# Kernel tuning notes

Hardware: AMD Instinct MI355X
Metric: run time of the kernel (lower is better)

Reference implementation:

```python
import jax, jax.numpy as jnp
import numpy as np

B, S, E, H = 2, 2048, 1024, 16
D = E // H  # head_dim = 64


def setup_inputs() -> dict:
    key = jax.random.key(0)
    ks = jax.random.split(key, 6)
    sc = 1.0 / np.sqrt(D)
    return {
        "x": jax.random.normal(ks[0], (B, S, E), dtype=jnp.float32),
        "Wq": jax.random.normal(ks[1], (D, D), dtype=jnp.float32) * sc,
        "Wk": jax.random.normal(ks[2], (D, D), dtype=jnp.float32) * sc,
        "Wv": jax.random.normal(ks[3], (D, D), dtype=jnp.float32) * sc,
        "Wo": jax.random.normal(ks[4], (E, E), dtype=jnp.float32) * (1.0 / np.sqrt(E)),
        "bo": jnp.zeros((E,), dtype=jnp.float32),
    }


def reference(x, Wq, Wk, Wv, Wo, bo):
    b, s, e = x.shape
    # split into heads: (B, H, S, D)
    xh = x.reshape(b, s, H, D).transpose(0, 2, 1, 3)
    # per-head linear projections (weights SHARED across heads); torch Linear: x @ W^T
    q = jnp.einsum('bhsd,ed->bhse', xh, Wq)
    k = jnp.einsum('bhsd,ed->bhse', xh, Wk)
    v = jnp.einsum('bhsd,ed->bhse', xh, Wv)
    # full attention matrix (B, H, S, S) — faithful to the naive original
    energy = jnp.einsum('bhqd,bhkd->bhqk', q, k)
    attn = jax.nn.softmax(energy / jnp.sqrt(jnp.asarray(D, x.dtype)), axis=-1)
    out = jnp.einsum('bhqk,bhkd->bhqd', attn, v)
    out = out.transpose(0, 2, 1, 3).reshape(b, s, e)
    return out @ Wo.T + bo
```

## Files before the change

### kernel.cpp

```cpp
#include <hip/hip_runtime.h>
#include <hip/hip_bf16.h>

#define B 2
#define S 2048
#define E 1024
#define H 16
#define D 64

typedef unsigned short ushort_t;
typedef __attribute__((ext_vector_type(8))) short bf16x8;
typedef __attribute__((ext_vector_type(4))) float f32x4;
typedef __attribute__((ext_vector_type(16))) float f32x16;

static __device__ __forceinline__ ushort_t f2bf(float f) {
    union { float f; unsigned u; } v; v.f = f;
    unsigned r = v.u + 0x7fffu + ((v.u >> 16) & 1u);
    return (ushort_t)(r >> 16);
}

#define MFMA(a, b, c)   __builtin_amdgcn_mfma_f32_16x16x32_bf16((a), (b), (c), 0, 0, 0)
#define MFMA32(a, b, c) __builtin_amdgcn_mfma_f32_32x32x16_bf16((a), (b), (c), 0, 0, 0)
#define PACKBF(hi, lo) __builtin_amdgcn_perm((hi), (lo), 0x07060302u)

__global__ __launch_bounds__(256) void cvt_w(
    const float* __restrict__ Wq, const float* __restrict__ Wk, const float* __restrict__ Wv,
    const float* __restrict__ Wo,
    ushort_t* __restrict__ wqb, ushort_t* __restrict__ wkb, ushort_t* __restrict__ wvb,
    ushort_t* __restrict__ wob)
{
    int gid = blockIdx.x, t = threadIdx.x;
    if (gid < 1024) {
        int i = gid * 1024 + t * 4;
        float4 f = *(const float4*)(Wo + i);
        ushort4 u; u.x = f2bf(f.x); u.y = f2bf(f.y); u.z = f2bf(f.z); u.w = f2bf(f.w);
        *(ushort4*)(wob + i) = u;
    } else {
        int idx = (gid - 1024) * 1024 + t * 4;
        int which = idx >> 12, off = idx & 4095;
        const float* src = (which == 0) ? Wq : (which == 1) ? Wk : Wv;
        ushort_t* dst    = (which == 0) ? wqb : (which == 1) ? wkb : wvb;
        float sc = (which == 0) ? 0.18033688011112042f : 1.0f;
        float4 f = *(const float4*)(src + off);
        ushort4 u; u.x = f2bf(f.x * sc); u.y = f2bf(f.y * sc);
        u.z = f2bf(f.z * sc); u.w = f2bf(f.w * sc);
        *(ushort4*)(dst + off) = u;
    }
}

__global__ __launch_bounds__(256) void qkv_proj(
    const float* __restrict__ x,
    const ushort_t* __restrict__ wq, const ushort_t* __restrict__ wk, const ushort_t* __restrict__ wv,
    ushort_t* __restrict__ q, ushort_t* __restrict__ k, ushort_t* __restrict__ vT)
{
    __shared__ ushort_t Xs[64][72];
    __shared__ ushort_t Wqs[64][72], Wks[64][72], Wvs[64][72];
    int t = threadIdx.x;
    int bh = blockIdx.y, b = bh >> 4, h = bh & 15;
    int s0 = blockIdx.x * 64;

    {
        int i = t >> 2, d0 = (t & 3) * 16;
        const float* xp = x + ((size_t)(b * S + s0 + i)) * E + h * D + d0;
        #pragma unroll
        for (int c = 0; c < 16; c += 4) {
            float4 f = *(const float4*)(xp + c);
            Xs[i][d0 + c + 0] = f2bf(f.x); Xs[i][d0 + c + 1] = f2bf(f.y);
            Xs[i][d0 + c + 2] = f2bf(f.z); Xs[i][d0 + c + 3] = f2bf(f.w);
        }
    }
    {
        int e = t >> 2, d0 = (t & 3) * 16;
        *(bf16x8*)&Wqs[e][d0]     = *(const bf16x8*)(wq + e * 64 + d0);
        *(bf16x8*)&Wqs[e][d0 + 8] = *(const bf16x8*)(wq + e * 64 + d0 + 8);
        *(bf16x8*)&Wks[e][d0]     = *(const bf16x8*)(wk + e * 64 + d0);
        *(bf16x8*)&Wks[e][d0 + 8] = *(const bf16x8*)(wk + e * 64 + d0 + 8);
        *(bf16x8*)&Wvs[e][d0]     = *(const bf16x8*)(wv + e * 64 + d0);
        *(bf16x8*)&Wvs[e][d0 + 8] = *(const bf16x8*)(wv + e * 64 + d0 + 8);
    }
    __syncthreads();

    int w = t >> 6, lane = t & 63, m = lane & 15, quad = lane >> 4;
    bf16x8 a0 = *(bf16x8*)&Xs[16 * w + m][quad * 8];
    bf16x8 a1 = *(bf16x8*)&Xs[16 * w + m][32 + quad * 8];
    f32x4 cq[4], ck[4], cv[4];
    #pragma unroll
    for (int nt = 0; nt < 4; nt++) { cq[nt] = (f32x4)0.f; ck[nt] = (f32x4)0.f; cv[nt] = (f32x4)0.f; }
    #pragma unroll
    for (int nt = 0; nt < 4; nt++) {
        bf16x8 b0, b1;
        b0 = *(bf16x8*)&Wqs[nt * 16 + m][quad * 8]; b1 = *(bf16x8*)&Wqs[nt * 16 + m][32 + quad * 8];
        cq[nt] = MFMA(a0, b0, cq[nt]); cq[nt] = MFMA(a1, b1, cq[nt]);
        b0 = *(bf16x8*)&Wks[nt * 16 + m][quad * 8]; b1 = *(bf16x8*)&Wks[nt * 16 + m][32 + quad * 8];
        ck[nt] = MFMA(a0, b0, ck[nt]); ck[nt] = MFMA(a1, b1, ck[nt]);
        b0 = *(bf16x8*)&Wvs[nt * 16 + m][quad * 8]; b1 = *(bf16x8*)&Wvs[nt * 16 + m][32 + quad * 8];
        cv[nt] = MFMA(a0, b0, cv[nt]); cv[nt] = MFMA(a1, b1, cv[nt]);
    }
    size_t base = (size_t)bh * S + s0;
    #pragma unroll
    for (int nt = 0; nt < 4; nt++)
        #pragma unroll
        for (int r = 0; r < 4; r++) {
            size_t idx = (base + 16 * w + quad * 4 + r) * D + nt * 16 + m;
            q[idx] = f2bf(cq[nt][r]);
            k[idx] = f2bf(ck[nt][r]);
        }
    __syncthreads();
    #pragma unroll
    for (int nt = 0; nt < 4; nt++)
        #pragma unroll
        for (int r = 0; r < 4; r++)
            Wvs[nt * 16 + m][16 * w + quad * 4 + r] = f2bf(cv[nt][r]);
    __syncthreads();
    {
        int d0 = t >> 2, sc = (t & 3) * 16;
        ushort_t* vp = vT + ((size_t)bh * D + d0) * S + s0 + sc;
        *(bf16x8*)(vp)     = *(bf16x8*)&Wvs[d0][sc];
        *(bf16x8*)(vp + 8) = *(bf16x8*)&Wvs[d0][sc + 8];
    }
}

__global__ __launch_bounds__(256) void flash_attn(
    const ushort_t* __restrict__ q, const ushort_t* __restrict__ k,
    const ushort_t* __restrict__ vT, ushort_t* __restrict__ ao)
{
    __shared__ ushort_t Ks[2][64][72];
    __shared__ ushort_t Vt[2][64][72];
    int t = threadIdx.x;
    int bh = blockIdx.y, b = bh >> 4, h = bh & 15;
    int q0 = blockIdx.x * 128;
    int w = t >> 6, lane = t & 63, l31 = lane & 31, half = lane >> 5;

    const ushort_t* qb = q + ((size_t)bh * S + q0) * D;
    const ushort_t* kb = k + (size_t)bh * S * D;
    const ushort_t* vb = vT + (size_t)bh * D * S;

    bf16x8 qf[4];
    {
        const ushort_t* qp = qb + (size_t)(w * 32 + l31) * D + half * 8;
        #pragma unroll
        for (int c = 0; c < 4; c++) qf[c] = *(const bf16x8*)(qp + c * 16);
    }

    f32x16 o0 = (f32x16)0.f, o1 = (f32x16)0.f;
    float2 ls2 = make_float2(0.f, 0.f);

    int sr = t >> 2, scc = (t & 3) * 16;
    bf16x8 kp0, kp1, vp0, vp1;

    {
        const ushort_t* kp = kb + (size_t)sr * D + scc;
        const ushort_t* vp = vb + (size_t)sr * S + scc;
        kp0 = *(const bf16x8*)(kp);     kp1 = *(const bf16x8*)(kp + 8);
        vp0 = *(const bf16x8*)(vp);     vp1 = *(const bf16x8*)(vp + 8);
        *(bf16x8*)&Ks[0][sr][scc]     = kp0;
        *(bf16x8*)&Ks[0][sr][scc + 8] = kp1;
        *(bf16x8*)&Vt[0][sr][scc]     = vp0;
        *(bf16x8*)&Vt[0][sr][scc + 8] = vp1;
    }
    __syncthreads();
    {
        const ushort_t* kp = kb + (size_t)(64 + sr) * D + scc;
        const ushort_t* vp = vb + (size_t)sr * S + 64 + scc;
        kp0 = *(const bf16x8*)(kp);     kp1 = *(const bf16x8*)(kp + 8);
        vp0 = *(const bf16x8*)(vp);     vp1 = *(const bf16x8*)(vp + 8);
    }

    const int NT = S / 64;
    for (int it = 0; it < NT; it++) {
        int p = it & 1;
        if (it + 1 < NT) {
            *(bf16x8*)&Ks[1 - p][sr][scc]     = kp0;
            *(bf16x8*)&Ks[1 - p][sr][scc + 8] = kp1;
            *(bf16x8*)&Vt[1 - p][sr][scc]     = vp0;
            *(bf16x8*)&Vt[1 - p][sr][scc + 8] = vp1;
        }
        if (it + 2 < NT) {
            int k0n = (it + 2) * 64;
            const ushort_t* kp = kb + (size_t)(k0n + sr) * D + scc;
            const ushort_t* vp = vb + (size_t)sr * S + k0n + scc;
            kp0 = *(const bf16x8*)(kp);     kp1 = *(const bf16x8*)(kp + 8);
            vp0 = *(const bf16x8*)(vp);     vp1 = *(const bf16x8*)(vp + 8);
        }

        union { unsigned u[4]; bf16x8 v; } pa[4];
        #pragma unroll
        for (int st = 0; st < 2; st++) {
            f32x16 e = (f32x16)0.f;
            #pragma unroll
            for (int c = 0; c < 4; c++) {
                bf16x8 ka = *(bf16x8*)&Ks[p][st * 32 + l31][c * 16 + half * 8];
                e = MFMA32(ka, qf[c], e);
            }
            unsigned pt[16];
            #pragma unroll
            for (int r = 0; r < 16; r += 2) {
                float pe0 = __builtin_amdgcn_exp2f(e[r]);
                float pe1 = __builtin_amdgcn_exp2f(e[r + 1]);
                ls2.x += pe0; ls2.y += pe1;
                pt[r]     = __float_as_uint(pe0);
                pt[r + 1] = __float_as_uint(pe1);
            }
            #pragma unroll
            for (int c2 = 0; c2 < 2; c2++) {
                int rb = c2 * 8;
                unsigned dA = PACKBF(pt[rb + 1], pt[rb + 0]);
                unsigned dB = PACKBF(pt[rb + 3], pt[rb + 2]);
                unsigned dC = PACKBF(pt[rb + 5], pt[rb + 4]);
                unsigned dD = PACKBF(pt[rb + 7], pt[rb + 6]);
                unsigned x1 = (unsigned)__shfl_xor((int)(half ? dA : dC), 32, 64);
                unsigned x2 = (unsigned)__shfl_xor((int)(half ? dB : dD), 32, 64);
                int kc = st * 2 + c2;
                pa[kc].u[0] = half ? x1 : dA;
                pa[kc].u[1] = half ? x2 : dB;
                pa[kc].u[2] = half ? dC : x1;
                pa[kc].u[3] = half ? dD : x2;
            }
        }

        #pragma unroll
        for (int kc = 0; kc < 4; kc++) {
            bf16x8 vf0 = *(bf16x8*)&Vt[p][l31][kc * 16 + half * 8];
            bf16x8 vf1 = *(bf16x8*)&Vt[p][32 + l31][kc * 16 + half * 8];
            o0 = MFMA32(pa[kc].v, vf0, o0);
            o1 = MFMA32(pa[kc].v, vf1, o1);
        }
        __syncthreads();
    }

    float lsum = ls2.x + ls2.y;
    float lfull = lsum + __shfl_xor(lsum, 32, 64);
    float inv = 1.001953125f / lfull;
    #pragma unroll
    for (int reg = 0; reg < 16; reg++) {
        int qrow = (reg & 3) + 8 * (reg >> 2) + 4 * half;
        float li = __shfl(inv, qrow, 64);
        int srow = q0 + w * 32 + qrow;
        size_t base = ((size_t)(b * S + srow)) * E + h * D + l31;
        ao[base]      = f2bf(o0[reg] * li);
        ao[base + 32] = f2bf(o1[reg] * li);
    }
}

__global__ __launch_bounds__(256) void out_proj(
    const ushort_t* __restrict__ A, const ushort_t* __restrict__ Wob,
    const float* __restrict__ bo, float* __restrict__ Y)
{
    __shared__ ushort_t As[2][128][72];
    __shared__ ushort_t Ws[2][64][72];
    int t = threadIdx.x;
    int n0 = blockIdx.x * 64, m0 = blockIdx.y * 128;
    int w = t >> 6, lane = t & 63, m = lane & 15, quad = lane >> 4;
    f32x4 acc[2][4];
    #pragma unroll
    for (int u = 0; u < 2; u++)
        #pragma unroll
        for (int nt = 0; nt < 4; nt++) acc[u][nt] = (f32x4)0.f;

    int ar = t >> 1, ac = (t & 1) * 32;
    int wr = t >> 2, wc = (t & 3) * 16;
    const ushort_t* apb = A + (size_t)(m0 + ar) * E + ac;
    const ushort_t* wpb = Wob + (size_t)(n0 + wr) * E + wc;

    bf16x8 arg[4], wrg[2];
    {
        #pragma unroll
        for (int i = 0; i < 4; i++) *(bf16x8*)&As[0][ar][ac + 8 * i] = *(const bf16x8*)(apb + 8 * i);
        *(bf16x8*)&Ws[0][wr][wc]     = *(const bf16x8*)(wpb);
        *(bf16x8*)&Ws[0][wr][wc + 8] = *(const bf16x8*)(wpb + 8);
    }
    __syncthreads();
    {
        #pragma unroll
        for (int i = 0; i < 4; i++) arg[i] = *(const bf16x8*)(apb + 64 + 8 * i);
        wrg[0] = *(const bf16x8*)(wpb + 64);
        wrg[1] = *(const bf16x8*)(wpb + 64 + 8);
    }

    const int KT = E / 64;
    for (int ks = 0; ks < KT; ks++) {
        int p = ks & 1;
        if (ks + 1 < KT) {
            #pragma unroll
            for (int i = 0; i < 4; i++) *(bf16x8*)&As[1 - p][ar][ac + 8 * i] = arg[i];
            *(bf16x8*)&Ws[1 - p][wr][wc]     = wrg[0];
            *(bf16x8*)&Ws[1 - p][wr][wc + 8] = wrg[1];
        }
        if (ks + 2 < KT) {
            int off = (ks + 2) * 64;
            #pragma unroll
            for (int i = 0; i < 4; i++) arg[i] = *(const bf16x8*)(apb + off + 8 * i);
            wrg[0] = *(const bf16x8*)(wpb + off);
            wrg[1] = *(const bf16x8*)(wpb + off + 8);
        }
        #pragma unroll
        for (int h2 = 0; h2 < 2; h2++) {
            bf16x8 af[2];
            af[0] = *(bf16x8*)&As[p][w * 32 + m][h2 * 32 + quad * 8];
            af[1] = *(bf16x8*)&As[p][w * 32 + 16 + m][h2 * 32 + quad * 8];
            #pragma unroll
            for (int nt = 0; nt < 4; nt++) {
                bf16x8 bfr = *(bf16x8*)&Ws[p][nt * 16 + m][h2 * 32 + quad * 8];
                acc[0][nt] = MFMA(af[0], bfr, acc[0][nt]);
                acc[1][nt] = MFMA(af[1], bfr, acc[1][nt]);
            }
        }
        __syncthreads();
    }
    #pragma unroll
    for (int u = 0; u < 2; u++)
        #pragma unroll
        for (int nt = 0; nt < 4; nt++)
            #pragma unroll
            for (int r = 0; r < 4; r++) {
                int row = m0 + w * 32 + u * 16 + quad * 4 + r;
                int col = n0 + nt * 16 + m;
                Y[(size_t)row * E + col] = acc[u][nt][r] + bo[col];
            }
}

extern "C" void kernel_launch(void* const* d_in, const int* in_sizes, int n_in,
                              void* d_out, int out_size, void* d_ws, size_t ws_size,
                              hipStream_t stream)
{
    const float* x  = (const float*)d_in[0];
    const float* Wq = (const float*)d_in[1];
    const float* Wk = (const float*)d_in[2];
    const float* Wv = (const float*)d_in[3];
    const float* Wo = (const float*)d_in[4];
    const float* bo = (const float*)d_in[5];
    float* Y = (float*)d_out;

    const size_t n = (size_t)B * H * S * D;
    ushort_t* qw  = (ushort_t*)d_ws;
    ushort_t* kw  = qw + n;
    ushort_t* vTw = kw + n;
    ushort_t* ao  = vTw + n;
    ushort_t* wob = ao + n;
    ushort_t* wqb = wob + (size_t)E * E;
    ushort_t* wkb = wqb + D * D;
    ushort_t* wvb = wkb + D * D;

    cvt_w<<<dim3(1024 + 12), 256, 0, stream>>>(Wq, Wk, Wv, Wo, wqb, wkb, wvb, wob);
    qkv_proj<<<dim3(S / 64, B * H), 256, 0, stream>>>(x, wqb, wkb, wvb, qw, kw, vTw);
    flash_attn<<<dim3(S / 128, B * H), 256, 0, stream>>>(qw, kw, vTw, ao);
    out_proj<<<dim3(E / 64, (B * S) / 128), 256, 0, stream>>>(ao, wob, bo, Y);
}
```

Measured before the change: 152.2 us.

## Restructure QKV projection: weights in registers, two seq tiles per block, vector stores

The QKV projection kernel now keeps the three weight matrices as MFMA A-operands in registers and streams two 64-row sequence tiles per block, swapping the operand roles so each lane writes four contiguous q/k elements with ushort4 stores instead of scalar ones. X is loaded and converted with 16-byte LDS writes, and V is transposed through a dedicated LDS buffer. The grid is halved, which amortizes the weight loads but reduces parallelism and adds extra barriers per tile. The projection is a small part of total time next to attention and the output projection.

```diff
diff --git a/kernel.cpp b/kernel.cpp
--- a/kernel.cpp
+++ b/kernel.cpp
@@ -16,6 +16,15 @@
     union { float f; unsigned u; } v; v.f = f;
     unsigned r = v.u + 0x7fffu + ((v.u >> 16) & 1u);
     return (ushort_t)(r >> 16);
+}
+
+static __device__ __forceinline__ bf16x8 load_cvt8(const float* p) {
+    float4 f0 = *(const float4*)(p);
+    float4 f1 = *(const float4*)(p + 4);
+    union { ushort_t s[8]; bf16x8 v; } u;
+    u.s[0] = f2bf(f0.x); u.s[1] = f2bf(f0.y); u.s[2] = f2bf(f0.z); u.s[3] = f2bf(f0.w);
+    u.s[4] = f2bf(f1.x); u.s[5] = f2bf(f1.y); u.s[6] = f2bf(f1.z); u.s[7] = f2bf(f1.w);
+    return u.v;
 }
 
 #define MFMA(a, b, c)   __builtin_amdgcn_mfma_f32_16x16x32_bf16((a), (b), (c), 0, 0, 0)
@@ -52,70 +61,70 @@
     const ushort_t* __restrict__ wq, const ushort_t* __restrict__ wk, const ushort_t* __restrict__ wv,
     ushort_t* __restrict__ q, ushort_t* __restrict__ k, ushort_t* __restrict__ vT)
 {
+    __shared__ ushort_t Ws3[3][64][72];
     __shared__ ushort_t Xs[64][72];
-    __shared__ ushort_t Wqs[64][72], Wks[64][72], Wvs[64][72];
+    __shared__ ushort_t Vls[64][72];
     int t = threadIdx.x;
     int bh = blockIdx.y, b = bh >> 4, h = bh & 15;
-    int s0 = blockIdx.x * 64;
-
-    {
-        int i = t >> 2, d0 = (t & 3) * 16;
-        const float* xp = x + ((size_t)(b * S + s0 + i)) * E + h * D + d0;
-        #pragma unroll
-        for (int c = 0; c < 16; c += 4) {
-            float4 f = *(const float4*)(xp + c);
-            Xs[i][d0 + c + 0] = f2bf(f.x); Xs[i][d0 + c + 1] = f2bf(f.y);
-            Xs[i][d0 + c + 2] = f2bf(f.z); Xs[i][d0 + c + 3] = f2bf(f.w);
-        }
-    }
+    int s00 = blockIdx.x * 128;
+
     {
         int e = t >> 2, d0 = (t & 3) * 16;
-        *(bf16x8*)&Wqs[e][d0]     = *(const bf16x8*)(wq + e * 64 + d0);
-        *(bf16x8*)&Wqs[e][d0 + 8] = *(const bf16x8*)(wq + e * 64 + d0 + 8);
-        *(bf16x8*)&Wks[e][d0]     = *(const bf16x8*)(wk + e * 64 + d0);
-        *(bf16x8*)&Wks[e][d0 + 8] = *(const bf16x8*)(wk + e * 64 + d0 + 8);
-        *(bf16x8*)&Wvs[e][d0]     = *(const bf16x8*)(wv + e * 64 + d0);
-        *(bf16x8*)&Wvs[e][d0 + 8] = *(const bf16x8*)(wv + e * 64 + d0 + 8);
+        *(bf16x8*)&Ws3[0][e][d0]     = *(const bf16x8*)(wq + e * 64 + d0);
+        *(bf16x8*)&Ws3[0][e][d0 + 8] = *(const bf16x8*)(wq + e * 64 + d0 + 8);
+        *(bf16x8*)&Ws3[1][e][d0]     = *(const bf16x8*)(wk + e * 64 + d0);
+        *(bf16x8*)&Ws3[1][e][d0 + 8] = *(const bf16x8*)(wk + e * 64 + d0 + 8);
+        *(bf16x8*)&Ws3[2][e][d0]     = *(const bf16x8*)(wv + e * 64 + d0);
+        *(bf16x8*)&Ws3[2][e][d0 + 8] = *(const bf16x8*)(wv + e * 64 + d0 + 8);
     }
     __syncthreads();
 
     int w = t >> 6, lane = t & 63, m = lane & 15, quad = lane >> 4;
-    bf16x8 a0 = *(bf16x8*)&Xs[16 * w + m][quad * 8];
-    bf16x8 a1 = *(bf16x8*)&Xs[16 * w + m][32 + quad * 8];
-    f32x4 cq[4], ck[4], cv[4];
-    #pragma unroll
-    for (int nt = 0; nt < 4; nt++) { cq[nt] = (f32x4)0.f; ck[nt] = (f32x4)0.f; cv[nt] = (f32x4)0.f; }
-    #pragma unroll
-    for (int nt = 0; nt < 4; nt++) {
-        bf16x8 b0, b1;
-        b0 = *(bf16x8*)&Wqs[nt * 16 + m][quad * 8]; b1 = *(bf16x8*)&Wqs[nt * 16 + m][32 + quad * 8];
-        cq[nt] = MFMA(a0, b0, cq[nt]); cq[nt] = MFMA(a1, b1, cq[nt]);
-        b0 = *(bf16x8*)&Wks[nt * 16 + m][quad * 8]; b1 = *(bf16x8*)&Wks[nt * 16 + m][32 + quad * 8];
-        ck[nt] = MFMA(a0, b0, ck[nt]); ck[nt] = MFMA(a1, b1, ck[nt]);
-        b0 = *(bf16x8*)&Wvs[nt * 16 + m][quad * 8]; b1 = *(bf16x8*)&Wvs[nt * 16 + m][32 + quad * 8];
-        cv[nt] = MFMA(a0, b0, cv[nt]); cv[nt] = MFMA(a1, b1, cv[nt]);
-    }
-    size_t base = (size_t)bh * S + s0;
-    #pragma unroll
-    for (int nt = 0; nt < 4; nt++)
-        #pragma unroll
-        for (int r = 0; r < 4; r++) {
-            size_t idx = (base + 16 * w + quad * 4 + r) * D + nt * 16 + m;
-            q[idx] = f2bf(cq[nt][r]);
-            k[idx] = f2bf(ck[nt][r]);
-        }
-    __syncthreads();
-    #pragma unroll
-    for (int nt = 0; nt < 4; nt++)
-        #pragma unroll
-        for (int r = 0; r < 4; r++)
-            Wvs[nt * 16 + m][16 * w + quad * 4 + r] = f2bf(cv[nt][r]);
-    __syncthreads();
-    {
-        int d0 = t >> 2, sc = (t & 3) * 16;
-        ushort_t* vp = vT + ((size_t)bh * D + d0) * S + s0 + sc;
-        *(bf16x8*)(vp)     = *(bf16x8*)&Wvs[d0][sc];
-        *(bf16x8*)(vp + 8) = *(bf16x8*)&Wvs[d0][sc + 8];
+    bf16x8 wa[3][2];
+    #pragma unroll
+    for (int m3 = 0; m3 < 3; m3++) {
+        wa[m3][0] = *(bf16x8*)&Ws3[m3][16 * w + m][quad * 8];
+        wa[m3][1] = *(bf16x8*)&Ws3[m3][16 * w + m][32 + quad * 8];
+    }
+
+    int xi = t >> 2, xd0 = (t & 3) * 16;
+    #pragma unroll
+    for (int st = 0; st < 2; st++) {
+        int s0 = s00 + st * 64;
+        __syncthreads();
+        {
+            const float* xp = x + ((size_t)(b * S + s0 + xi)) * E + h * D + xd0;
+            *(bf16x8*)&Xs[xi][xd0]     = load_cvt8(xp);
+            *(bf16x8*)&Xs[xi][xd0 + 8] = load_cvt8(xp + 8);
+        }
+        __syncthreads();
+
+        size_t base = (size_t)bh * S + s0;
+        #pragma unroll
+        for (int nt = 0; nt < 4; nt++) {
+            bf16x8 xb0 = *(bf16x8*)&Xs[nt * 16 + m][quad * 8];
+            bf16x8 xb1 = *(bf16x8*)&Xs[nt * 16 + m][32 + quad * 8];
+            f32x4 cq = (f32x4)0.f, ck = (f32x4)0.f, cv = (f32x4)0.f;
+            cq = MFMA(wa[0][0], xb0, cq); cq = MFMA(wa[0][1], xb1, cq);
+            ck = MFMA(wa[1][0], xb0, ck); ck = MFMA(wa[1][1], xb1, ck);
+            cv = MFMA(wa[2][0], xb0, cv); cv = MFMA(wa[2][1], xb1, cv);
+            size_t rowoff = (base + nt * 16 + m) * D + 16 * w + quad * 4;
+            ushort4 uq, uk;
+            uq.x = f2bf(cq[0]); uq.y = f2bf(cq[1]); uq.z = f2bf(cq[2]); uq.w = f2bf(cq[3]);
+            uk.x = f2bf(ck[0]); uk.y = f2bf(ck[1]); uk.z = f2bf(ck[2]); uk.w = f2bf(ck[3]);
+            *(ushort4*)(q + rowoff) = uq;
+            *(ushort4*)(k + rowoff) = uk;
+            #pragma unroll
+            for (int r = 0; r < 4; r++)
+                Vls[16 * w + quad * 4 + r][nt * 16 + m] = f2bf(cv[r]);
+        }
+        __syncthreads();
+        {
+            int d0 = t >> 2, sc = (t & 3) * 16;
+            ushort_t* vp = vT + ((size_t)bh * D + d0) * S + s0 + sc;
+            *(bf16x8*)(vp)     = *(bf16x8*)&Vls[d0][sc];
+            *(bf16x8*)(vp + 8) = *(bf16x8*)&Vls[d0][sc + 8];
+        }
     }
 }
 
@@ -341,7 +350,7 @@
     ushort_t* wvb = wkb + D * D;
 
     cvt_w<<<dim3(1024 + 12), 256, 0, stream>>>(Wq, Wk, Wv, Wo, wqb, wkb, wvb, wob);
-    qkv_proj<<<dim3(S / 64, B * H), 256, 0, stream>>>(x, wqb, wkb, wvb, qw, kw, vTw);
+    qkv_proj<<<dim3(S / 128, B * H), 256, 0, stream>>>(x, wqb, wkb, wvb, qw, kw, vTw);
     flash_attn<<<dim3(S / 128, B * H), 256, 0, stream>>>(qw, kw, vTw, ao);
     out_proj<<<dim3(E / 64, (B * S) / 128), 256, 0, stream>>>(ao, wob, bo, Y);
 }
```

New measurement: 153.8 us. No clear change (+1.1%).
